# Kernel tuning notes

Hardware: AMD Instinct MI355X
Metric: run time of the kernel (lower is better)

## Reference

```python
import jax, jax.numpy as jnp
import numpy as np

# Static model dims
B, N, EMB, D, H, HD, L, NC = 1, 4096, 1024, 512, 8, 64, 2, 2
# Per-head local neighborhood sizes (round(pi*local_k^2) in the original, static here)
K_PER_HEAD = (32, 48, 64, 80, 96, 112, 128, 160)
SCALE = float(np.sqrt(HD))  # sigma_sq = sqrt(head_dim) in the original


def _ln(x, g, b, eps=1e-5):
    m = x.mean(-1, keepdims=True)
    v = ((x - m) ** 2).mean(-1, keepdims=True)
    return (x - m) * jax.lax.rsqrt(v + eps) * g + b


def _gather(a, idx):
    # a: [B, N, ...], idx: [B, N, K] -> [B, N, K, ...] (per-batch row gather, as k_h[range(B), indices])
    return jax.vmap(lambda ah, ih: ah[ih])(a, idx)


def setup_inputs() -> dict:
    key = jax.random.key(0)
    ks = iter(jax.random.split(key, 48))
    w = lambda shape: 0.02 * jax.random.normal(next(ks), shape, jnp.float32)
    return {
        "x": jax.random.normal(next(ks), (B, N, EMB), jnp.float32),
        "distance": 10.0 * jax.random.uniform(next(ks), (B, N, N), jnp.float32),
        "indices": jax.random.randint(next(ks), (B, N, K_PER_HEAD[-1]), 0, N, jnp.int32),
        "row": jax.random.randint(next(ks), (B, N), 0, 128, jnp.int32),
        "col": jax.random.randint(next(ks), (B, N), 0, 128, jnp.int32),
        # adapter (ResidualFullyConnected, simplified: linear proj + 1 residual layer)
        "adapter_w": w((EMB, D)), "adapter_b": jnp.zeros((D,), jnp.float32),
        "res_w": w((D, D)), "res_b": jnp.zeros((D,), jnp.float32),
        # per-block params, stacked over depth L
        "ln1_g": jnp.ones((L, D), jnp.float32), "ln1_b": jnp.zeros((L, D), jnp.float32),
        "qkv_w": w((L, D, 3 * D)), "qkv_b": jnp.zeros((L, 3 * D), jnp.float32),
        "proj_w": w((L, D, D)), "proj_b": jnp.zeros((L, D), jnp.float32),
        "ln2_g": jnp.ones((L, D), jnp.float32), "ln2_b": jnp.zeros((L, D), jnp.float32),
        "fc1_w": w((L, D, 4 * D)), "fc1_b": jnp.zeros((L, 4 * D), jnp.float32),
        "fc2_w": w((L, 4 * D, D)), "fc2_b": jnp.zeros((L, D), jnp.float32),
        # per-head decay rate parameter (DecayNetwork lambda_p); reparam = softplus
        "lam": 0.5 + w((L, H)),
        "lnf_g": jnp.ones((D,), jnp.float32), "lnf_b": jnp.zeros((D,), jnp.float32),
        "head_w": w((D, NC)), "head_b": jnp.zeros((NC,), jnp.float32),
    }


def _forward(x, distance, indices, adapter_w, adapter_b, res_w, res_b,
             ln1_g, ln1_b, qkv_w, qkv_b, proj_w, proj_b,
             ln2_g, ln2_b, fc1_w, fc1_b, fc2_w, fc2_b,
             lam, lnf_g, lnf_b, head_w, head_b):
    h = x @ adapter_w + adapter_b
    h = h + jax.nn.relu(h @ res_w + res_b)  # residual adapter layer
    for l in range(L):
        # --- spatial multi-head attention with per-head KNN window + decay log-bias ---
        xa = _ln(h, ln1_g[l], ln1_b[l])
        qkv = (xa @ qkv_w[l] + qkv_b[l]).reshape(B, N, 3, H, HD).transpose(2, 0, 3, 1, 4)
        q, k, v = qkv[0], qkv[1], qkv[2]          # [B,H,N,d]
        qn = jnp.sum(q * q, -1)                    # [B,H,N]  |q|^2
        kn = jnp.sum(k * k, -1)                    # [B,H,N]  |k|^2
        heads = []
        for hh in range(H):
            Kh = K_PER_HEAD[hh]
            idx = indices[:, :, :Kh]               # [B,N,Kh] nearest neighbors
            ksel = _gather(k[:, hh], idx)          # [B,N,Kh,d]
            vsel = _gather(v[:, hh], idx)          # [B,N,Kh,d]
            knsel = _gather(kn[:, hh], idx)        # [B,N,Kh]
            attn = jnp.einsum('bnd,bnkd->bnk', q[:, hh], ksel) / SCALE
            attn = attn - 0.5 * (qn[:, hh][..., None] + knsel) / SCALE  # norm correction
            dsel = jnp.take_along_axis(distance, idx, axis=-1)          # [B,N,Kh]
            decay = jnp.exp(-jax.nn.softplus(lam[l, hh]) * dsel) + 1e-6
            attn = jax.nn.softmax(attn + jnp.log(decay), axis=-1)
            heads.append(jnp.einsum('bnk,bnkd->bnd', attn, vsel))
        xo = jnp.stack(heads, 2).reshape(B, N, D)  # [B,N,H,d] -> [B,N,D]
        h = h + (xo @ proj_w[l] + proj_b[l])
        # --- MLP ---
        xm = _ln(h, ln2_g[l], ln2_b[l])
        h = h + (jax.nn.gelu(xm @ fc1_w[l] + fc1_b[l]) @ fc2_w[l] + fc2_b[l])
    h = _ln(h, lnf_g, lnf_b, eps=1e-6)
    return h.mean(axis=1) @ head_w + head_b  # avg pool + head -> [B, num_classes]


def reference(x, distance, indices, row, col, adapter_w, adapter_b, res_w, res_b,
              ln1_g, ln1_b, qkv_w, qkv_b, proj_w, proj_b,
              ln2_g, ln2_b, fc1_w, fc1_b, fc2_w, fc2_b,
              lam, lnf_g, lnf_b, head_w, head_b):
    # row/col are carried as metadata in the original forward and unused by the math
    return _forward(x, distance, indices, adapter_w, adapter_b, res_w, res_b,
                    ln1_g, ln1_b, qkv_w, qkv_b, proj_w, proj_b,
                    ln2_g, ln2_b, fc1_w, fc1_b, fc2_w, fc2_b,
                    lam, lnf_g, lnf_b, head_w, head_b)
```

## Files before the change

kernel.cpp:

```cpp
#include <hip/hip_runtime.h>
#include <hip/hip_bf16.h>

#define NTOK 4096
#define EMB 1024
#define DMODEL 512
#define NHEAD 8
#define NLAYER 2
#define NCLS 2
#define KMAX 160

typedef __attribute__((ext_vector_type(8))) short bf16x8;
typedef __attribute__((ext_vector_type(4))) float f32x4;

__device__ inline unsigned short f2b(float f) {
    unsigned u = __float_as_uint(f);
    u = u + 0x7FFFu + ((u >> 16) & 1u);
    return (unsigned short)(u >> 16);
}
__device__ inline float b2f(unsigned short s) {
    return __uint_as_float((unsigned)s << 16);
}

__device__ inline float dot2bf(unsigned a, unsigned b, float c) {
    float d;
    asm("v_dot2_f32_bf16 %0, %1, %2, %3" : "=v"(d) : "v"(a), "v"(b), "v"(c));
    return d;
}

__device__ inline float wsum(float v) {
    for (int o = 32; o > 0; o >>= 1) v += __shfl_xor(v, o, 64);
    return v;
}
__device__ inline float wmax(float v) {
    for (int o = 32; o > 0; o >>= 1) v = fmaxf(v, __shfl_xor(v, o, 64));
    return v;
}

typedef __attribute__((address_space(3))) unsigned lds_u32_t;
typedef __attribute__((address_space(1))) const unsigned glb_u32_t;
__device__ inline void gload16(const void* g, void* l) {
    __builtin_amdgcn_global_load_lds((glb_u32_t*)(unsigned long long)g,
                                     (lds_u32_t*)(unsigned)(unsigned long long)l,
                                     16, 0, 0);
}

__device__ const int g_s0cnt[8]  = {576, 448, 720, 144, 365, 490, 460, 159};
__device__ const int g_s0h[8]    = {7, 7, 6, 6, 5, 4, 3, 2};
__device__ const int g_s0base[8] = {0, 576, 160, 880, 659, 534, 564, 865};
__device__ const int g_s1cnt[8]  = {0, 160, 0, 659, 534, 564, 865, 1024};
__device__ const int g_s1h[8]    = {0, 6, 0, 5, 4, 3, 2, 1};
#define ATTN_BLOCKS (2207 * 8)

struct WSeg { const float* src; unsigned short* dst; int K; int N; int tile0; };
struct WSegs { WSeg s[6]; };

__global__ __launch_bounds__(256) void wcvt_all_k(WSegs segs)
{
    __shared__ unsigned short tile[64][72];
    int t0 = blockIdx.x;
    int si = 0;
#pragma unroll
    for (int i = 1; i < 6; i++) if (t0 >= segs.s[i].tile0) si = i;
    const float* src0 = segs.s[si].src;
    unsigned short* dst0 = segs.s[si].dst;
    int K = segs.s[si].K, N = segs.s[si].N;
    int lt = t0 - segs.s[si].tile0;
    int tx = K >> 6, ty = N >> 6;
    int per = tx * ty;
    int l = lt / per, rr = lt - l * per;
    int k0 = (rr % tx) << 6, n0 = (rr / tx) << 6;
    size_t ls = (size_t)K * N * l;
    const float* Wl = src0 + ls;
    unsigned short* Wtl = dst0 + ls;

    int t = threadIdx.x;
    int kl = t >> 2, nb = (t & 3) * 16;
    const float* src = Wl + (size_t)(k0 + kl) * N + n0 + nb;
#pragma unroll
    for (int i = 0; i < 4; i++) {
        float4 v = *(const float4*)(src + 4 * i);
        tile[nb + 4 * i + 0][kl] = f2b(v.x);
        tile[nb + 4 * i + 1][kl] = f2b(v.y);
        tile[nb + 4 * i + 2][kl] = f2b(v.z);
        tile[nb + 4 * i + 3][kl] = f2b(v.w);
    }
    __syncthreads();
    int nl = t >> 2, ks = (t & 3) * 16;
    unsigned short* dst = Wtl + (size_t)(n0 + nl) * K + k0 + ks;
    *(uint4*)dst = *(const uint4*)&tile[nl][ks];
    *(uint4*)(dst + 8) = *(const uint4*)&tile[nl][ks + 8];
}

__global__ __launch_bounds__(256) void xcvt_k(const float* __restrict__ X,
                                              unsigned short* __restrict__ Xb)
{
    int i = (blockIdx.x * 256 + threadIdx.x) * 8;
    float4 a = *(const float4*)(X + i);
    float4 b = *(const float4*)(X + i + 4);
    unsigned short o[8];
    o[0] = f2b(a.x); o[1] = f2b(a.y); o[2] = f2b(a.z); o[3] = f2b(a.w);
    o[4] = f2b(b.x); o[5] = f2b(b.y); o[6] = f2b(b.z); o[7] = f2b(b.w);
    *(uint4*)(Xb + i) = *(const uint4*)o;
}

__global__ __launch_bounds__(256) void dsel_k(const float* __restrict__ distance,
                                              const int* __restrict__ indices,
                                              float* __restrict__ dsel)
{
    int n = blockIdx.x, t = threadIdx.x;
    if (t < KMAX) {
        int idx = indices[(size_t)n * KMAX + t];
        dsel[(size_t)n * KMAX + t] = distance[(size_t)n * NTOK + idx];
    }
}

template <int BM, int BN, int WM, int WN, int MODE>
__global__ __launch_bounds__(256) void mgemm_k(
    const unsigned short* __restrict__ A, const unsigned short* __restrict__ Wt,
    const float* __restrict__ bias, const float* __restrict__ resid,
    float* __restrict__ Cf, unsigned short* __restrict__ Cb,
    float* __restrict__ knout,
    int M, int N, int K)
{
    constexpr int SM = BM / WM;
    constexpr int SN = BN / WN;
    constexpr int MR = SM / 16;
    constexpr int NR = SN / 16;

    __shared__ unsigned short Asl[2][BM * 32];
    __shared__ unsigned short Bsl[2][BN * 32];

    int tid = threadIdx.x;
    int bm = blockIdx.x * BM, bn = blockIdx.y * BN;
    int lane = tid & 63, wid = tid >> 6;
    int wm = wid / WN, wn = wid % WN;
    int l15 = lane & 15, l4 = lane >> 4;

    f32x4 acc[MR][NR] = {};

    int sr = tid >> 2;
    int scl = (((tid & 3) ^ ((sr >> 1) & 3))) * 8;
    int dst_off = sr * 32 + (tid & 3) * 8;
    const unsigned short* Asrc = A  + (size_t)(bm + sr) * K + scl;
    const unsigned short* Bsrc = Wt + (size_t)(bn + sr) * K + scl;

    int arow = wm * SM + l15;
    int brow = wn * SN + l15;
    int aoff0 = arow * 32 + (l4 ^ ((arow >> 1) & 3)) * 8;
    int boff0 = brow * 32 + (l4 ^ ((brow >> 1) & 3)) * 8;

    auto stage = [&](int buf, int k0) {
#pragma unroll
        for (int i = 0; i < BM / 64; i++)
            gload16(Asrc + (size_t)(i * 64) * K + k0, &Asl[buf][i * 64 * 32 + dst_off]);
#pragma unroll
        for (int i = 0; i < BN / 64; i++)
            gload16(Bsrc + (size_t)(i * 64) * K + k0, &Bsl[buf][i * 64 * 32 + dst_off]);
    };

    int nt = K / 32;
    stage(0, 0);
    __syncthreads();
    int cur = 0;
    for (int t = 0; t < nt; t++) {
        if (t + 1 < nt) stage(cur ^ 1, (t + 1) * 32);
        bf16x8 af[MR], bfr[NR];
#pragma unroll
        for (int mr = 0; mr < MR; mr++) af[mr] = *(const bf16x8*)&Asl[cur][aoff0 + mr * 16 * 32];
#pragma unroll
        for (int nr = 0; nr < NR; nr++) bfr[nr] = *(const bf16x8*)&Bsl[cur][boff0 + nr * 16 * 32];
#pragma unroll
        for (int mr = 0; mr < MR; mr++)
#pragma unroll
            for (int nr = 0; nr < NR; nr++)
                acc[mr][nr] = __builtin_amdgcn_mfma_f32_16x16x32_bf16(af[mr], bfr[nr], acc[mr][nr], 0, 0, 0);
        __syncthreads();
        cur ^= 1;
    }

#pragma unroll
    for (int mr = 0; mr < MR; mr++) {
#pragma unroll
        for (int nr = 0; nr < NR; nr++) {
            int col = bn + wn * SN + nr * 16 + l15;
            float bcol = bias[col];
#pragma unroll
            for (int r = 0; r < 4; r++) {
                int row = bm + wm * SM + mr * 16 + l4 * 4 + r;
                size_t off = (size_t)row * N + col;
                float v = acc[mr][nr][r] + bcol;
                if (MODE == 0) {
                    Cf[off] = v;
                } else if (MODE == 1) {
                    Cf[off] = resid[off] + fmaxf(v, 0.f);
                } else if (MODE == 2) {
                    float t3 = tanhf(0.7978845608028654f * (v + 0.044715f * v * v * v));
                    Cb[off] = f2b(0.5f * v * (1.f + t3));
                } else if (MODE == 3) {
                    Cf[off] = resid[off] + v;
                } else if (MODE == 4) {
                    Cf[off] = v;
                    Cb[off] = f2b(v);
                } else {
                    Cb[off] = f2b(v);
                }
            }
        }
    }

    if (MODE == 5) {
        int cbase = bn + wn * SN;
        if (cbase >= 512 && cbase < 1024) {
            int hh = (cbase - 512) >> 6;
#pragma unroll
            for (int mr = 0; mr < MR; mr++) {
#pragma unroll
                for (int r = 0; r < 4; r++) {
                    float p = 0.f;
#pragma unroll
                    for (int nr = 0; nr < NR; nr++) {
                        float v = acc[mr][nr][r] + bias[cbase + nr * 16 + l15];
                        p += v * v;
                    }
                    p += __shfl_xor(p, 1, 64);
                    p += __shfl_xor(p, 2, 64);
                    p += __shfl_xor(p, 4, 64);
                    p += __shfl_xor(p, 8, 64);
                    if (l15 == 0) {
                        int row = bm + wm * SM + mr * 16 + l4 * 4 + r;
                        knout[row * NHEAD + hh] = p;
                    }
                }
            }
        }
    }
}

template <int OUTB>
__global__ __launch_bounds__(256) void ln_k(
    const float* __restrict__ X, const float* __restrict__ g,
    const float* __restrict__ bta, void* __restrict__ Yv, float eps)
{
    int row = blockIdx.x;
    int tid = threadIdx.x;
    const float* xr = X + (size_t)row * DMODEL;
    float v0 = xr[tid], v1 = xr[tid + 256];
    __shared__ float red[8];
    float s = wsum(v0 + v1);
    int wid = tid >> 6, lane = tid & 63;
    if (lane == 0) red[wid] = s;
    __syncthreads();
    float m = (red[0] + red[1] + red[2] + red[3]) * (1.f / DMODEL);
    float d0 = v0 - m, d1 = v1 - m;
    float sq = wsum(d0 * d0 + d1 * d1);
    if (lane == 0) red[4 + wid] = sq;
    __syncthreads();
    float var = (red[4] + red[5] + red[6] + red[7]) * (1.f / DMODEL);
    float rs = 1.0f / sqrtf(var + eps);
    float y0 = d0 * rs * g[tid] + bta[tid];
    float y1 = d1 * rs * g[tid + 256] + bta[tid + 256];
    if (OUTB) {
        unsigned short* Y = (unsigned short*)Yv;
        Y[(size_t)row * DMODEL + tid] = f2b(y0);
        Y[(size_t)row * DMODEL + tid + 256] = f2b(y1);
    } else {
        float* Y = (float*)Yv;
        Y[(size_t)row * DMODEL + tid] = y0;
        Y[(size_t)row * DMODEL + tid + 256] = y1;
    }
}

__global__ __launch_bounds__(256) void attn_k(
    const unsigned short* __restrict__ qkv,
    const float* __restrict__ kn,
    const int* __restrict__ indices, const float* __restrict__ dsel,
    const float* __restrict__ lam, unsigned short* __restrict__ xo, int layer)
{
    int xcd = blockIdx.x & 7;
    int t = blockIdx.x >> 3;
    int hh, blk;
    int c0 = g_s0cnt[xcd];
    if (t < c0) {
        hh = g_s0h[xcd]; blk = g_s0base[xcd] + t;
    } else {
        t -= c0;
        int c1 = g_s1cnt[xcd];
        if (t < c1) {
            hh = g_s1h[xcd]; blk = t;
        } else if (xcd == 7 && t - c1 < 1024) {
            hh = 0; blk = t - c1;
        } else {
            return;
        }
    }

    int wid = threadIdx.x >> 6, lane = threadIdx.x & 63;
    int n = blk * 4 + wid;
    int Kh = 32 + 16 * hh + (hh == 7 ? 16 : 0);

    __shared__ __align__(16) unsigned qsp[4][32];
    __shared__ float asc[4][KMAX];
    __shared__ int   sidx[4][KMAX];

    const unsigned short* qrow = qkv + (size_t)n * 1536 + hh * 64;
    float qd = b2f(qrow[lane]);
    if (lane < 32) qsp[wid][lane] = ((const unsigned*)qrow)[lane];
    float qn2 = wsum(qd * qd);
    float sp = log1pf(expf(lam[layer * NHEAD + hh]));

    const int* irow = indices + (size_t)n * KMAX;
    const float* drow = dsel + (size_t)n * KMAX;

    int sub = lane & 3, grp = lane >> 2;
    const uint4* qp = (const uint4*)&qsp[wid][0];
    uint4 qa = qp[sub], qb = qp[4 + sub];

    int iters = Kh >> 4;
    for (int it = 0; it < iters; it++) {
        int kk = it * 16 + grp;
        int idx = irow[kk];
        const uint4* krow = (const uint4*)(qkv + (size_t)idx * 1536 + 512 + hh * 64);
        uint4 ka = krow[sub];
        uint4 kb = krow[4 + sub];
        float d0 = 0.f, d1 = 0.f, d2 = 0.f, d3 = 0.f;
        d0 = dot2bf(ka.x, qa.x, d0); d1 = dot2bf(ka.y, qa.y, d1);
        d2 = dot2bf(ka.z, qa.z, d2); d3 = dot2bf(ka.w, qa.w, d3);
        d0 = dot2bf(kb.x, qb.x, d0); d1 = dot2bf(kb.y, qb.y, d1);
        d2 = dot2bf(kb.z, qb.z, d2); d3 = dot2bf(kb.w, qb.w, d3);
        float dp = (d0 + d1) + (d2 + d3);
        dp += __shfl_xor(dp, 1, 64);
        dp += __shfl_xor(dp, 2, 64);
        if (sub == 0) {
            asc[wid][kk] = dp;
            sidx[wid][kk] = idx;
        }
    }

    float s0 = -1e30f, s1 = -1e30f, s2 = -1e30f;
    {
        int kk = lane;
        if (kk < Kh) {
            float dp = asc[wid][kk];
            float knv = kn[sidx[wid][kk] * NHEAD + hh];
            float dec = expf(-sp * drow[kk]) + 1e-6f;
            s0 = (dp - 0.5f * (qn2 + knv)) * 0.125f + logf(dec);
        }
        kk = lane + 64;
        if (kk < Kh) {
            float dp = asc[wid][kk];
            float knv = kn[sidx[wid][kk] * NHEAD + hh];
            float dec = expf(-sp * drow[kk]) + 1e-6f;
            s1 = (dp - 0.5f * (qn2 + knv)) * 0.125f + logf(dec);
        }
        kk = lane + 128;
        if (kk < Kh) {
            float dp = asc[wid][kk];
            float knv = kn[sidx[wid][kk] * NHEAD + hh];
            float dec = expf(-sp * drow[kk]) + 1e-6f;
            s2 = (dp - 0.5f * (qn2 + knv)) * 0.125f + logf(dec);
        }
    }
    float mx = wmax(fmaxf(fmaxf(s0, s1), s2));
    float e0 = (s0 > -1e29f) ? expf(s0 - mx) : 0.f;
    float e1 = (s1 > -1e29f) ? expf(s1 - mx) : 0.f;
    float e2 = (s2 > -1e29f) ? expf(s2 - mx) : 0.f;
    float se = wsum(e0 + e1 + e2);
    float inv = 1.f / se;
    if (lane < Kh)       asc[wid][lane]       = e0 * inv;
    if (lane + 64 < Kh)  asc[wid][lane + 64]  = e1 * inv;
    if (lane + 128 < Kh) asc[wid][lane + 128] = e2 * inv;

    int g = lane >> 3, q = lane & 7;
    const uint4* vb = (const uint4*)(qkv + 1024 + hh * 64 + q * 8);
    float a8[8] = {};
    int k0 = 0;
    int kmain = Kh & ~31;
    for (; k0 < kmain; k0 += 32) {
        int ii[4]; float aa[4]; uint4 vv[4];
#pragma unroll
        for (int u = 0; u < 4; u++) {
            int kk = k0 + u * 8 + g;
            ii[u] = sidx[wid][kk];
            aa[u] = asc[wid][kk];
        }
#pragma unroll
        for (int u = 0; u < 4; u++) vv[u] = vb[(size_t)ii[u] * 192];
#pragma unroll
        for (int u = 0; u < 4; u++) {
            const unsigned short* vp = (const unsigned short*)&vv[u];
#pragma unroll
            for (int d = 0; d < 8; d++) a8[d] += aa[u] * b2f(vp[d]);
        }
    }
    if (Kh & 16) {
        int ii[2]; float aa[2]; uint4 vv[2];
#pragma unroll
        for (int u = 0; u < 2; u++) {
            int kk = k0 + u * 8 + g;
            ii[u] = sidx[wid][kk];
            aa[u] = asc[wid][kk];
        }
#pragma unroll
        for (int u = 0; u < 2; u++) vv[u] = vb[(size_t)ii[u] * 192];
#pragma unroll
        for (int u = 0; u < 2; u++) {
            const unsigned short* vp = (const unsigned short*)&vv[u];
#pragma unroll
            for (int d = 0; d < 8; d++) a8[d] += aa[u] * b2f(vp[d]);
        }
    }
#pragma unroll
    for (int d = 0; d < 8; d++) {
        a8[d] += __shfl_xor(a8[d], 8, 64);
        a8[d] += __shfl_xor(a8[d], 16, 64);
        a8[d] += __shfl_xor(a8[d], 32, 64);
    }
    if (lane < 8) {
        unsigned o[4];
#pragma unroll
        for (int p = 0; p < 4; p++)
            o[p] = ((unsigned)f2b(a8[2 * p + 1]) << 16) | (unsigned)f2b(a8[2 * p]);
        *(uint4*)(xo + (size_t)n * DMODEL + hh * 64 + lane * 8) = *(uint4*)o;
    }
}

__global__ __launch_bounds__(512) void colpart_k(const float* __restrict__ Y, float* __restrict__ part)
{
    int c = threadIdx.x;
    int blk = blockIdx.x;
    const float* p = Y + (size_t)blk * 16 * DMODEL + c;
    float s = 0.f;
#pragma unroll
    for (int r = 0; r < 16; r++) s += p[r * DMODEL];
    part[blk * DMODEL + c] = s;
}

__global__ __launch_bounds__(512) void finhead_k(
    const float* __restrict__ part, const float* __restrict__ head_w,
    const float* __restrict__ head_b, float* __restrict__ out)
{
    __shared__ float mv[DMODEL];
    int c = threadIdx.x;
    float s = 0.f;
    for (int i = 0; i < 256; i++) s += part[i * DMODEL + c];
    mv[c] = s * (1.f / NTOK);
    __syncthreads();
    if (c < 64) {
        float a0 = 0.f, a1 = 0.f;
        for (int d = c; d < DMODEL; d += 64) {
            float m = mv[d];
            a0 += m * head_w[d * NCLS + 0];
            a1 += m * head_w[d * NCLS + 1];
        }
        a0 = wsum(a0);
        a1 = wsum(a1);
        if (c == 0) { out[0] = a0 + head_b[0]; out[1] = a1 + head_b[1]; }
    }
}

extern "C" void kernel_launch(void* const* d_in, const int* in_sizes, int n_in,
                              void* d_out, int out_size, void* d_ws, size_t ws_size,
                              hipStream_t stream)
{
    const float* x        = (const float*)d_in[0];
    const float* distance = (const float*)d_in[1];
    const int*   indices  = (const int*)d_in[2];
    const float* adapter_w = (const float*)d_in[5];
    const float* adapter_b = (const float*)d_in[6];
    const float* res_w     = (const float*)d_in[7];
    const float* res_b     = (const float*)d_in[8];
    const float* ln1_g     = (const float*)d_in[9];
    const float* ln1_b     = (const float*)d_in[10];
    const float* qkv_w     = (const float*)d_in[11];
    const float* qkv_b     = (const float*)d_in[12];
    const float* proj_w    = (const float*)d_in[13];
    const float* proj_b    = (const float*)d_in[14];
    const float* ln2_g     = (const float*)d_in[15];
    const float* ln2_b     = (const float*)d_in[16];
    const float* fc1_w     = (const float*)d_in[17];
    const float* fc1_b     = (const float*)d_in[18];
    const float* fc2_w     = (const float*)d_in[19];
    const float* fc2_b     = (const float*)d_in[20];
    const float* lam       = (const float*)d_in[21];
    const float* lnf_g     = (const float*)d_in[22];
    const float* lnf_b     = (const float*)d_in[23];
    const float* head_w    = (const float*)d_in[24];
    const float* head_b    = (const float*)d_in[25];
    float* out = (float*)d_out;

    char* wsb = (char*)d_ws;
    float* h   = (float*)(wsb);
    float* h0  = (float*)(wsb + (8u << 20));
    float* dsel = (float*)(wsb + (8u << 20));
    char* shared = wsb + (16u << 20);
    unsigned short* xb    = (unsigned short*)shared;
    unsigned short* qkvbb = (unsigned short*)shared;
    unsigned short* fc1b  = (unsigned short*)shared;
    unsigned short* adapter_wt = (unsigned short*)(shared + (8u << 20));
    unsigned short* res_wt     = (unsigned short*)(shared + (9u << 20));
    unsigned short* lnb  = (unsigned short*)(wsb + (40u << 20));
    unsigned short* h0b  = lnb;
    unsigned short* xob  = (unsigned short*)(wsb + (44u << 20));
    unsigned short* qkv_wt = (unsigned short*)(wsb + (48u << 20));
    unsigned short* proj_wt = (unsigned short*)(wsb + (51u << 20));
    unsigned short* fc1_wt  = (unsigned short*)(wsb + (52u << 20));
    unsigned short* fc2_wt  = (unsigned short*)(wsb + (56u << 20));
    float* kn   = (float*)(wsb + (60u << 20));
    float* part = (float*)(wsb + (60u << 20) + (1u << 18));

    dim3 blk(256);

    xcvt_k<<<(NTOK * EMB) / 2048, blk, 0, stream>>>(x, xb);
    {
        WSegs segs;
        segs.s[0] = { adapter_w, adapter_wt, EMB,    DMODEL, 0 };
        segs.s[1] = { res_w,     res_wt,     DMODEL, DMODEL, 128 };
        segs.s[2] = { qkv_w,     qkv_wt,     DMODEL, 1536,   192 };
        segs.s[3] = { proj_w,    proj_wt,    DMODEL, DMODEL, 576 };
        segs.s[4] = { fc1_w,     fc1_wt,     DMODEL, 2048,   704 };
        segs.s[5] = { fc2_w,     fc2_wt,     2048,   DMODEL, 1216 };
        wcvt_all_k<<<1728, blk, 0, stream>>>(segs);
    }

    mgemm_k<64, 64, 2, 2, 4><<<dim3(NTOK / 64, DMODEL / 64), blk, 0, stream>>>(
        xb, adapter_wt, adapter_b, nullptr, h0, h0b, nullptr, NTOK, DMODEL, EMB);
    mgemm_k<64, 64, 2, 2, 1><<<dim3(NTOK / 64, DMODEL / 64), blk, 0, stream>>>(
        h0b, res_wt, res_b, h0, h, nullptr, nullptr, NTOK, DMODEL, DMODEL);

    dsel_k<<<NTOK, blk, 0, stream>>>(distance, indices, dsel);

    for (int l = 0; l < NLAYER; l++) {
        ln_k<1><<<NTOK, blk, 0, stream>>>(h, ln1_g + l * DMODEL, ln1_b + l * DMODEL, lnb, 1e-5f);
        mgemm_k<64, 128, 2, 2, 5><<<dim3(NTOK / 64, 1536 / 128), blk, 0, stream>>>(
            lnb, qkv_wt + (size_t)l * 1536 * DMODEL, qkv_b + l * 1536, nullptr,
            nullptr, qkvbb, kn, NTOK, 1536, DMODEL);
        attn_k<<<ATTN_BLOCKS, blk, 0, stream>>>(qkvbb, kn, indices, dsel, lam, xob, l);
        mgemm_k<64, 64, 2, 2, 3><<<dim3(NTOK / 64, DMODEL / 64), blk, 0, stream>>>(
            xob, proj_wt + (size_t)l * DMODEL * DMODEL, proj_b + l * DMODEL, h,
            h, nullptr, nullptr, NTOK, DMODEL, DMODEL);
        ln_k<1><<<NTOK, blk, 0, stream>>>(h, ln2_g + l * DMODEL, ln2_b + l * DMODEL, lnb, 1e-5f);
        mgemm_k<64, 128, 2, 2, 2><<<dim3(NTOK / 64, 2048 / 128), blk, 0, stream>>>(
            lnb, fc1_wt + (size_t)l * 2048 * DMODEL, fc1_b + l * 2048, nullptr,
            nullptr, fc1b, nullptr, NTOK, 2048, DMODEL);
        mgemm_k<64, 64, 2, 2, 3><<<dim3(NTOK / 64, DMODEL / 64), blk, 0, stream>>>(
            fc1b, fc2_wt + (size_t)l * DMODEL * 2048, fc2_b + l * DMODEL, h,
            h, nullptr, nullptr, NTOK, DMODEL, 2048);
    }

    ln_k<0><<<NTOK, blk, 0, stream>>>(h, lnf_g, lnf_b, h0, 1e-6f);
    colpart_k<<<256, 512, 0, stream>>>(h0, part);
    finhead_k<<<1, 512, 0, stream>>>(part, head_w, head_b, out);
}
```

Before: 354.1 us.

## Merge prep kernels, widen GEMM K-tile to 64, prefetch attention keys, simplify decay log

The x conversion and weight conversion are folded into one launch. The bf16 GEMM now stages 64-wide K slices with an XOR swizzle, which halves the number of barrier iterations. Attention prefetches the next key row group before computing the current dot products. log(exp(-sp*d)+1e-6) is replaced by -sp*d, which drops the epsilon and can differ slightly when decay underflows.

```diff
diff --git a/kernel.cpp b/kernel.cpp
--- a/kernel.cpp
+++ b/kernel.cpp
@@ -52,19 +52,29 @@
 #define ATTN_BLOCKS (2207 * 8)
 
 struct WSeg { const float* src; unsigned short* dst; int K; int N; int tile0; };
-struct WSegs { WSeg s[6]; };
-
-__global__ __launch_bounds__(256) void wcvt_all_k(WSegs segs)
+struct Prep { WSeg s[6]; const float* x; unsigned short* xb; int xtile0; };
+
+__global__ __launch_bounds__(256) void prep_k(Prep p)
 {
     __shared__ unsigned short tile[64][72];
     int t0 = blockIdx.x;
+    if (t0 >= p.xtile0) {
+        int i = ((t0 - p.xtile0) * 256 + threadIdx.x) * 8;
+        float4 a = *(const float4*)(p.x + i);
+        float4 b = *(const float4*)(p.x + i + 4);
+        unsigned short o[8];
+        o[0] = f2b(a.x); o[1] = f2b(a.y); o[2] = f2b(a.z); o[3] = f2b(a.w);
+        o[4] = f2b(b.x); o[5] = f2b(b.y); o[6] = f2b(b.z); o[7] = f2b(b.w);
+        *(uint4*)(p.xb + i) = *(const uint4*)o;
+        return;
+    }
     int si = 0;
 #pragma unroll
-    for (int i = 1; i < 6; i++) if (t0 >= segs.s[i].tile0) si = i;
-    const float* src0 = segs.s[si].src;
-    unsigned short* dst0 = segs.s[si].dst;
-    int K = segs.s[si].K, N = segs.s[si].N;
-    int lt = t0 - segs.s[si].tile0;
+    for (int i = 1; i < 6; i++) if (t0 >= p.s[i].tile0) si = i;
+    const float* src0 = p.s[si].src;
+    unsigned short* dst0 = p.s[si].dst;
+    int K = p.s[si].K, N = p.s[si].N;
+    int lt = t0 - p.s[si].tile0;
     int tx = K >> 6, ty = N >> 6;
     int per = tx * ty;
     int l = lt / per, rr = lt - l * per;
@@ -91,18 +101,6 @@
     *(uint4*)(dst + 8) = *(const uint4*)&tile[nl][ks + 8];
 }
 
-__global__ __launch_bounds__(256) void xcvt_k(const float* __restrict__ X,
-                                              unsigned short* __restrict__ Xb)
-{
-    int i = (blockIdx.x * 256 + threadIdx.x) * 8;
-    float4 a = *(const float4*)(X + i);
-    float4 b = *(const float4*)(X + i + 4);
-    unsigned short o[8];
-    o[0] = f2b(a.x); o[1] = f2b(a.y); o[2] = f2b(a.z); o[3] = f2b(a.w);
-    o[4] = f2b(b.x); o[5] = f2b(b.y); o[6] = f2b(b.z); o[7] = f2b(b.w);
-    *(uint4*)(Xb + i) = *(const uint4*)o;
-}
-
 __global__ __launch_bounds__(256) void dsel_k(const float* __restrict__ distance,
                                               const int* __restrict__ indices,
                                               float* __restrict__ dsel)
@@ -127,8 +125,8 @@
     constexpr int MR = SM / 16;
     constexpr int NR = SN / 16;
 
-    __shared__ unsigned short Asl[2][BM * 32];
-    __shared__ unsigned short Bsl[2][BN * 32];
+    __shared__ unsigned short Asl[2][BM * 64];
+    __shared__ unsigned short Bsl[2][BN * 64];
 
     int tid = threadIdx.x;
     int bm = blockIdx.x * BM, bn = blockIdx.y * BN;
@@ -138,42 +136,48 @@
 
     f32x4 acc[MR][NR] = {};
 
-    int sr = tid >> 2;
-    int scl = (((tid & 3) ^ ((sr >> 1) & 3))) * 8;
-    int dst_off = sr * 32 + (tid & 3) * 8;
-    const unsigned short* Asrc = A  + (size_t)(bm + sr) * K + scl;
-    const unsigned short* Bsrc = Wt + (size_t)(bn + sr) * K + scl;
-
-    int arow = wm * SM + l15;
-    int brow = wn * SN + l15;
-    int aoff0 = arow * 32 + (l4 ^ ((arow >> 1) & 3)) * 8;
-    int boff0 = brow * 32 + (l4 ^ ((brow >> 1) & 3)) * 8;
-
     auto stage = [&](int buf, int k0) {
 #pragma unroll
-        for (int i = 0; i < BM / 64; i++)
-            gload16(Asrc + (size_t)(i * 64) * K + k0, &Asl[buf][i * 64 * 32 + dst_off]);
-#pragma unroll
-        for (int i = 0; i < BN / 64; i++)
-            gload16(Bsrc + (size_t)(i * 64) * K + k0, &Bsl[buf][i * 64 * 32 + dst_off]);
+        for (int i = 0; i < BM / 32; i++) {
+            int ci = i * 256 + tid;
+            int r = ci >> 3, c = ci & 7;
+            gload16(A + (size_t)(bm + r) * K + k0 + ((c ^ (r & 7)) * 8),
+                    &Asl[buf][ci * 8]);
+        }
+#pragma unroll
+        for (int i = 0; i < BN / 32; i++) {
+            int ci = i * 256 + tid;
+            int r = ci >> 3, c = ci & 7;
+            gload16(Wt + (size_t)(bn + r) * K + k0 + ((c ^ (r & 7)) * 8),
+                    &Bsl[buf][ci * 8]);
+        }
     };
 
-    int nt = K / 32;
+    int nt = K / 64;
     stage(0, 0);
     __syncthreads();
     int cur = 0;
     for (int t = 0; t < nt; t++) {
-        if (t + 1 < nt) stage(cur ^ 1, (t + 1) * 32);
-        bf16x8 af[MR], bfr[NR];
-#pragma unroll
-        for (int mr = 0; mr < MR; mr++) af[mr] = *(const bf16x8*)&Asl[cur][aoff0 + mr * 16 * 32];
-#pragma unroll
-        for (int nr = 0; nr < NR; nr++) bfr[nr] = *(const bf16x8*)&Bsl[cur][boff0 + nr * 16 * 32];
-#pragma unroll
-        for (int mr = 0; mr < MR; mr++)
-#pragma unroll
-            for (int nr = 0; nr < NR; nr++)
-                acc[mr][nr] = __builtin_amdgcn_mfma_f32_16x16x32_bf16(af[mr], bfr[nr], acc[mr][nr], 0, 0, 0);
+        if (t + 1 < nt) stage(cur ^ 1, (t + 1) * 64);
+#pragma unroll
+        for (int ks = 0; ks < 2; ks++) {
+            bf16x8 af[MR], bfr[NR];
+#pragma unroll
+            for (int mr = 0; mr < MR; mr++) {
+                int ar = wm * SM + mr * 16 + l15;
+                af[mr] = *(const bf16x8*)&Asl[cur][ar * 64 + ((((ks << 2) | l4) ^ (ar & 7)) * 8)];
+            }
+#pragma unroll
+            for (int nr = 0; nr < NR; nr++) {
+                int br = wn * SN + nr * 16 + l15;
+                bfr[nr] = *(const bf16x8*)&Bsl[cur][br * 64 + ((((ks << 2) | l4) ^ (br & 7)) * 8)];
+            }
+#pragma unroll
+            for (int mr = 0; mr < MR; mr++)
+#pragma unroll
+                for (int nr = 0; nr < NR; nr++)
+                    acc[mr][nr] = __builtin_amdgcn_mfma_f32_16x16x32_bf16(af[mr], bfr[nr], acc[mr][nr], 0, 0, 0);
+        }
         __syncthreads();
         cur ^= 1;
     }
@@ -316,12 +320,17 @@
     uint4 qa = qp[sub], qb = qp[4 + sub];
 
     int iters = Kh >> 4;
+    int idxn = irow[grp];
+    const uint4* krn = (const uint4*)(qkv + (size_t)idxn * 1536 + 512 + hh * 64);
+    uint4 kan = krn[sub], kbn = krn[4 + sub];
     for (int it = 0; it < iters; it++) {
-        int kk = it * 16 + grp;
-        int idx = irow[kk];
-        const uint4* krow = (const uint4*)(qkv + (size_t)idx * 1536 + 512 + hh * 64);
-        uint4 ka = krow[sub];
-        uint4 kb = krow[4 + sub];
+        int idxc = idxn;
+        uint4 ka = kan, kb = kbn;
+        if (it + 1 < iters) {
+            idxn = irow[(it + 1) * 16 + grp];
+            const uint4* kr = (const uint4*)(qkv + (size_t)idxn * 1536 + 512 + hh * 64);
+            kan = kr[sub]; kbn = kr[4 + sub];
+        }
         float d0 = 0.f, d1 = 0.f, d2 = 0.f, d3 = 0.f;
         d0 = dot2bf(ka.x, qa.x, d0); d1 = dot2bf(ka.y, qa.y, d1);
         d2 = dot2bf(ka.z, qa.z, d2); d3 = dot2bf(ka.w, qa.w, d3);
@@ -331,8 +340,9 @@
         dp += __shfl_xor(dp, 1, 64);
         dp += __shfl_xor(dp, 2, 64);
         if (sub == 0) {
+            int kk = it * 16 + grp;
             asc[wid][kk] = dp;
-            sidx[wid][kk] = idx;
+            sidx[wid][kk] = idxc;
         }
     }
 
@@ -340,24 +350,18 @@
     {
         int kk = lane;
         if (kk < Kh) {
-            float dp = asc[wid][kk];
             float knv = kn[sidx[wid][kk] * NHEAD + hh];
-            float dec = expf(-sp * drow[kk]) + 1e-6f;
-            s0 = (dp - 0.5f * (qn2 + knv)) * 0.125f + logf(dec);
+            s0 = (asc[wid][kk] - 0.5f * (qn2 + knv)) * 0.125f - sp * drow[kk];
         }
         kk = lane + 64;
         if (kk < Kh) {
-            float dp = asc[wid][kk];
             float knv = kn[sidx[wid][kk] * NHEAD + hh];
-            float dec = expf(-sp * drow[kk]) + 1e-6f;
-            s1 = (dp - 0.5f * (qn2 + knv)) * 0.125f + logf(dec);
+            s1 = (asc[wid][kk] - 0.5f * (qn2 + knv)) * 0.125f - sp * drow[kk];
         }
         kk = lane + 128;
         if (kk < Kh) {
-            float dp = asc[wid][kk];
             float knv = kn[sidx[wid][kk] * NHEAD + hh];
-            float dec = expf(-sp * drow[kk]) + 1e-6f;
-            s2 = (dp - 0.5f * (qn2 + knv)) * 0.125f + logf(dec);
+            s2 = (asc[wid][kk] - 0.5f * (qn2 + knv)) * 0.125f - sp * drow[kk];
         }
     }
     float mx = wmax(fmaxf(fmaxf(s0, s1), s2));
@@ -510,16 +514,16 @@
 
     dim3 blk(256);
 
-    xcvt_k<<<(NTOK * EMB) / 2048, blk, 0, stream>>>(x, xb);
     {
-        WSegs segs;
-        segs.s[0] = { adapter_w, adapter_wt, EMB,    DMODEL, 0 };
-        segs.s[1] = { res_w,     res_wt,     DMODEL, DMODEL, 128 };
-        segs.s[2] = { qkv_w,     qkv_wt,     DMODEL, 1536,   192 };
-        segs.s[3] = { proj_w,    proj_wt,    DMODEL, DMODEL, 576 };
-        segs.s[4] = { fc1_w,     fc1_wt,     DMODEL, 2048,   704 };
-        segs.s[5] = { fc2_w,     fc2_wt,     2048,   DMODEL, 1216 };
-        wcvt_all_k<<<1728, blk, 0, stream>>>(segs);
+        Prep p;
+        p.s[0] = { adapter_w, adapter_wt, EMB,    DMODEL, 0 };
+        p.s[1] = { res_w,     res_wt,     DMODEL, DMODEL, 128 };
+        p.s[2] = { qkv_w,     qkv_wt,     DMODEL, 1536,   192 };
+        p.s[3] = { proj_w,    proj_wt,    DMODEL, DMODEL, 576 };
+        p.s[4] = { fc1_w,     fc1_wt,     DMODEL, 2048,   704 };
+        p.s[5] = { fc2_w,     fc2_wt,     2048,   DMODEL, 1216 };
+        p.x = x; p.xb = xb; p.xtile0 = 1728;
+        prep_k<<<1728 + (NTOK * EMB) / 2048, blk, 0, stream>>>(p);
     }
 
     mgemm_k<64, 64, 2, 2, 4><<<dim3(NTOK / 64, DMODEL / 64), blk, 0, stream>>>(
```

Result: faster. 330.2 us (-6.7%).
